# Kernel optimization log

Measured on AMD Instinct MI355X. Metric: run time of the kernel, lower is better.

Reference implementation:

```python
import jax, jax.numpy as jnp
import numpy as np

B, N, T = 512, 24, 25
IN, L, H, OUT = 8, 64, 256, 128


def quat_mul(q, r):
    w1, x1, y1, z1 = jnp.split(q, 4, -1)
    w2, x2, y2, z2 = jnp.split(r, 4, -1)
    return jnp.concatenate([
        w1 * w2 - x1 * x2 - y1 * y2 - z1 * z2,
        w1 * x2 + x1 * w2 + y1 * z2 - z1 * y2,
        w1 * y2 - x1 * z2 + y1 * w2 + z1 * x2,
        w1 * z2 + x1 * y2 - y1 * x2 + z1 * w2], -1)


def node_linear(x, W, b, G):
    # per-node weights [N,F,O], then graph-influence mixing G[N,N]
    y = jnp.einsum('bnf,nfo->bno', x, W) + b
    return jnp.einsum('mn,bno->bmo', G, y)


def graph_linear(x, W, b, G):
    # shared weights [F,O], then graph-influence mixing
    y = jnp.einsum('bnf,fo->bno', x, W) + b
    return jnp.einsum('mn,bno->bmo', G, y)


def lstm_step(x, h, c, Wx, Wh, b, G):
    gates = jnp.einsum('bnf,nfo->bno', x, Wx) + jnp.einsum('bnf,nfo->bno', h, Wh) + b
    gates = jnp.einsum('mn,bno->bmo', G, gates)
    i, f, g, o = jnp.split(gates, 4, -1)
    c = jax.nn.sigmoid(f) * c + jax.nn.sigmoid(i) * jnp.tanh(g)
    h = jax.nn.sigmoid(o) * jnp.tanh(c)
    return h, c


def _p(key, shape, scale):
    return jax.random.normal(key, shape, jnp.float32) * scale


def setup_inputs() -> dict:
    key = jax.random.key(0)
    ks = jax.random.split(key, 20)
    in0 = L + IN
    inp = {
        'x': jax.random.normal(ks[0], (B, 1, N, IN), jnp.float32),
        'enc': jax.random.normal(ks[1], (B, 1, N, H), jnp.float32),
        'z': jax.random.normal(ks[2], (B, 1, N, L), jnp.float32),
        'y': jax.random.normal(ks[3], (B, T, N, 4), jnp.float32),
        'G': jnp.eye(N, dtype=jnp.float32) + 0.02 * jax.random.normal(ks[4], (N, N), jnp.float32),
        'Wx0': _p(ks[5], (N, in0, 4 * OUT), in0 ** -0.5),
        'Wh0': _p(ks[6], (N, OUT, 4 * OUT), OUT ** -0.5),
        'b0': jnp.zeros((N, 4 * OUT), jnp.float32),
        'Wx1': _p(ks[7], (N, OUT, 4 * OUT), OUT ** -0.5),
        'Wh1': _p(ks[8], (N, OUT, 4 * OUT), OUT ** -0.5),
        'b1': jnp.zeros((N, 4 * OUT), jnp.float32),
        'fc_W': _p(ks[9], (N, OUT, OUT), OUT ** -0.5),
        'fc_b': jnp.zeros((N, OUT), jnp.float32),
        'fc2_W': _p(ks[10], (N, OUT, OUT), OUT ** -0.5),
        'fc2_b': jnp.zeros((N, OUT), jnp.float32),
        'ih1_W': _p(ks[11], (H, OUT), H ** -0.5),
        'ih1_b': jnp.zeros((OUT,), jnp.float32),
        'ih2_W': _p(ks[12], (H, OUT), H ** -0.5),
        'ih2_b': jnp.zeros((OUT,), jnp.float32),
        'loc_W': _p(ks[13], (OUT, 3), OUT ** -0.5),
        'loc_b': jnp.zeros((3,), jnp.float32),
        'logz_W': _p(ks[14], (OUT, 4), OUT ** -0.5),
        'logz_b': jnp.zeros((4,), jnp.float32),
    }
    return inp


def reference(x, enc, z, y, G, Wx0, Wh0, b0, Wx1, Wh1, b1, fc_W, fc_b, fc2_W, fc2_b,
              ih1_W, ih1_b, ih2_W, ih2_b, loc_W, loc_b, logz_W, logz_b):
    # eval mode: dropout = identity, no teacher forcing (y unused); rnn2/xi2 are dead code.
    xs, zs, encs = x[:, 0], z[:, 0], enc[:, 0]          # [B,N,*]
    h0 = graph_linear(encs, ih1_W, ih1_b, G)            # shared initial h for both layers
    c0 = graph_linear(encs, ih2_W, ih2_b, G)            # shared initial c for both layers
    loc_start0 = xs[..., :4]
    xi0 = jnp.concatenate([zs, xs], -1)                 # [B,N,L+IN]

    def step(carry, _):
        xi, loc_start, h1, c1, h2, c2 = carry
        h1, c1 = lstm_step(xi, h1, c1, Wx0, Wh0, b0, G)
        h2, c2 = lstm_step(h1, h2, c2, Wx1, Wh1, b1, G)
        yi = jnp.tanh(h2)
        yi1 = jnp.tanh(node_linear(yi, fc_W, fc_b, G))
        yi2 = jnp.tanh(node_linear(yi, fc2_W, fc2_b, G))
        loc3 = graph_linear(yi1, loc_W, loc_b, G)       # [B,N,3]
        log_Z = graph_linear(yi2, logz_W, logz_b, G)    # [B,N,4]
        w = jnp.ones(loc3.shape[:-1] + (1,), loc3.dtype)
        loc4 = jnp.concatenate([w, loc3], -1)
        loc_d = loc4 * jax.lax.rsqrt(jnp.sum(loc4 * loc4, -1, keepdims=True))  # validate
        loc = quat_mul(loc_start, loc_d)                # state_representation.sum
        xi_next = jnp.concatenate([zs, loc, loc_d], -1)
        return (xi_next, loc, h1, c1, h2, c2), (loc, log_Z)

    _, (locs, logzs) = jax.lax.scan(step, (xi0, loc_start0, h0, c0, h0, c0), None, length=T)
    out = jnp.moveaxis(locs, 0, 1)[:, :, None]          # [B,T,1,N,4]
    out_log_diag = jnp.moveaxis(logzs, 0, 1)[:, :, None]
    return out, out_log_diag
```

## Files before the change

kernel.cpp:

```cpp
#include <hip/hip_runtime.h>
#include <math.h>

#define Bsz 512
#define Nn  24
#define Tt  25

typedef _Float16 f16;
typedef _Float16 f16x8 __attribute__((ext_vector_type(8)));
typedef _Float16 f16x4 __attribute__((ext_vector_type(4)));
typedef float f32x4 __attribute__((ext_vector_type(4)));

template <int FN>
__global__ __launch_bounds__(256) void gemm_mfma(
    const f16* __restrict__ Act, const float* __restrict__ Act32, int Ka,
    const f16* __restrict__ W, size_t wstride,
    const float* __restrict__ bias, int bstride,
    const f16* __restrict__ base16,
    f16* __restrict__ Y, int O)
{
    const int BN = FN * 32;
    const int n  = blockIdx.z;
    const int o0 = blockIdx.x * 64;
    const int b0 = blockIdx.y * BN;
    const int tid  = threadIdx.x;
    const int wave = tid >> 6, lane = tid & 63;
    const int wm = (wave >> 1) * 32;
    const int wn = (wave & 1) * FN * 16;
    const int m16 = lane & 15, quad = lane >> 4;

    __shared__ __attribute__((aligned(16))) f16 sW[64][72];
    __shared__ __attribute__((aligned(16))) f16 sB[BN][72];

    const f16* Wn = W + (size_t)n * wstride;
    f32x4 acc[2][FN] = {};
    const int r = tid >> 3, cc = (tid & 7) * 8;

    for (int k0 = 0; k0 < Ka; k0 += 64) {
        for (int row = r; row < 64; row += 32)
            *(f16x8*)&sW[row][cc] = *(const f16x8*)&Wn[(size_t)(o0 + row) * Ka + k0 + cc];
        if (Act) {
            for (int row = r; row < BN; row += 32)
                *(f16x8*)&sB[row][cc] = *(const f16x8*)&Act[((size_t)(b0 + row) * Nn + n) * Ka + k0 + cc];
        } else {
            for (int row = r; row < BN; row += 32) {
                const float* src = &Act32[((size_t)(b0 + row) * Nn + n) * Ka + k0 + cc];
                f16x8 v;
#pragma unroll
                for (int u = 0; u < 8; u++) v[u] = (f16)src[u];
                *(f16x8*)&sB[row][cc] = v;
            }
        }
        __syncthreads();
#pragma unroll
        for (int kk = 0; kk < 64; kk += 32) {
            f16x8 af[2], bf[FN];
#pragma unroll
            for (int i = 0; i < 2; i++)
                af[i] = *(const f16x8*)&sW[wm + i * 16 + m16][kk + quad * 8];
#pragma unroll
            for (int j = 0; j < FN; j++)
                bf[j] = *(const f16x8*)&sB[wn + j * 16 + m16][kk + quad * 8];
#pragma unroll
            for (int i = 0; i < 2; i++)
#pragma unroll
                for (int j = 0; j < FN; j++)
                    acc[i][j] = __builtin_amdgcn_mfma_f32_16x16x32_f16(af[i], bf[j], acc[i][j], 0, 0, 0);
        }
        __syncthreads();
    }
#pragma unroll
    for (int i = 0; i < 2; i++) {
        const int orow = o0 + wm + i * 16 + quad * 4;
        float4 bv = make_float4(0.f, 0.f, 0.f, 0.f);
        if (bias) bv = *(const float4*)&bias[(size_t)n * bstride + orow];
#pragma unroll
        for (int j = 0; j < FN; j++) {
            const int bcol = b0 + wn + j * 16 + m16;
            size_t yi = ((size_t)bcol * Nn + n) * (size_t)O + orow;
            float v0 = acc[i][j][0] + bv.x;
            float v1 = acc[i][j][1] + bv.y;
            float v2 = acc[i][j][2] + bv.z;
            float v3 = acc[i][j][3] + bv.w;
            if (base16) {
                f16x4 bb = *(const f16x4*)&base16[yi];
                v0 += (float)bb[0]; v1 += (float)bb[1];
                v2 += (float)bb[2]; v3 += (float)bb[3];
            }
            f16x4 o4; o4[0] = (f16)v0; o4[1] = (f16)v1; o4[2] = (f16)v2; o4[3] = (f16)v3;
            *(f16x4*)&Y[yi] = o4;
        }
    }
}

__global__ __launch_bounds__(256) void prep_w01(
    const float* __restrict__ Wx0, const float* __restrict__ Wh0,
    const float* __restrict__ Wx1, const float* __restrict__ Wh1,
    f16* __restrict__ Wz, f16* __restrict__ Wt0, f16* __restrict__ W2ext,
    f16* __restrict__ W8)
{
    size_t idx = (size_t)blockIdx.x * 256 + threadIdx.x;
    const size_t nz = (size_t)Nn * 512 * 64;
    const size_t n0 = (size_t)Nn * 512 * 192;
    const size_t n2 = (size_t)Nn * 1024 * 256;
    const size_t n8 = (size_t)Nn * 8 * 512;
    if (idx < nz) {
        int k = idx & 63; int o = (idx >> 6) & 511; int n = (int)(idx >> 15);
        Wz[idx] = (f16)Wx0[((size_t)n * 72 + k) * 512 + o];
    } else if (idx < nz + n0) {
        size_t i2 = idx - nz;
        int k = (int)(i2 % 192);
        size_t no = i2 / 192;
        int o = (int)(no & 511); int n = (int)(no >> 9);
        float v = 0.f;
        if (k < 8) v = Wx0[((size_t)n * 72 + 64 + k) * 512 + o];
        else if (k < 136) v = Wh0[((size_t)n * 128 + (k - 8)) * 512 + o];
        Wt0[i2] = (f16)v;
    } else if (idx < nz + n0 + n2) {
        size_t i3 = idx - nz - n0;
        int k = (int)(i3 & 255);
        size_t no = i3 >> 8;
        int o = (int)(no & 1023); int n = (int)(no >> 10);
        float v;
        if (o < 512) v = (k < 128) ? Wx1[((size_t)n * 128 + k) * 512 + o]
                                   : Wh1[((size_t)n * 128 + (k - 128)) * 512 + o];
        else         v = (k < 128) ? Wh0[((size_t)n * 128 + k) * 512 + (o - 512)] : 0.f;
        W2ext[i3] = (f16)v;
    } else if (idx < nz + n0 + n2 + n8) {
        size_t i4 = idx - nz - n0 - n2;
        int o = (int)(i4 & 511);
        size_t ko = i4 >> 9;
        int k = (int)(ko & 7); int n = (int)(ko >> 3);
        W8[i4] = (f16)Wx0[((size_t)n * 72 + 64 + k) * 512 + o];
    }
}

__global__ __launch_bounds__(256) void prep_wf(
    const float* __restrict__ fcW, const float* __restrict__ fc2W,
    f16* __restrict__ Wtf)
{
    size_t idx = (size_t)blockIdx.x * 256 + threadIdx.x;
    if (idx >= (size_t)Nn * 256 * 128) return;
    int k = (int)(idx & 127);
    size_t no = idx >> 7;
    int o = (int)(no & 255); int n = (int)(no >> 8);
    float v = (o < 128) ? fcW[((size_t)n * 128 + k) * 128 + o]
                        : fc2W[((size_t)n * 128 + k) * 128 + (o - 128)];
    Wtf[idx] = (f16)v;
}

__global__ __launch_bounds__(256) void prep_wi(
    const float* __restrict__ ih1W, const float* __restrict__ ih2W,
    const float* __restrict__ ih1b, const float* __restrict__ ih2b,
    const float* __restrict__ fcb, const float* __restrict__ fc2b,
    const float* __restrict__ b1,
    f16* __restrict__ Wti, float* __restrict__ bi, float* __restrict__ bcat,
    float* __restrict__ bcat2)
{
    int idx = blockIdx.x * 256 + threadIdx.x;
    int k = idx & 255, o = idx >> 8;
    Wti[idx] = (f16)((o < 128) ? ih1W[(size_t)k * 128 + o] : ih2W[(size_t)k * 128 + (o - 128)]);
    if (idx < 256) bi[idx] = (idx < 128) ? ih1b[idx] : ih2b[idx - 128];
    if (idx < Nn * 256) {
        int n = idx >> 8, oo = idx & 255;
        bcat[idx] = (oo < 128) ? fcb[n * 128 + oo] : fc2b[n * 128 + (oo - 128)];
    }
    if (idx < Nn * 1024) {
        int n = idx >> 10, oo = idx & 1023;
        bcat2[idx] = (oo < 512) ? b1[n * 512 + oo] : 0.f;
    }
}

__global__ __launch_bounds__(256) void init_xi(
    const float* __restrict__ x, f16* __restrict__ xi2, float* __restrict__ ls)
{
    size_t idx = (size_t)blockIdx.x * 256 + threadIdx.x;
    const size_t total = (size_t)Bsz * Nn * 192;
    if (idx < total) {
        size_t bn = idx / 192;
        int k = (int)(idx - bn * 192);
        if (k < 8) xi2[idx] = (f16)x[bn * 8 + k];
        else if (k >= 136) xi2[idx] = (f16)0.f;
    }
    if (idx < (size_t)Bsz * Nn * 4) {
        size_t bn = idx >> 2;
        ls[idx] = x[bn * 8 + (idx & 3)];
    }
}

__global__ __launch_bounds__(256) void mix_init(
    const f16* __restrict__ Yhc, const float* __restrict__ G,
    f16* __restrict__ xi2, f16* __restrict__ l2cat,
    float* __restrict__ c1, float* __restrict__ c2)
{
    const int b = blockIdx.x;
    const int tid = threadIdx.x;
    __shared__ float sY[6144], sG[576];
    for (int i = tid; i < 576; i += 256) sG[i] = G[i];
    for (int v = tid; v < 768; v += 256) {
        int c8 = (v & 31) * 8, n = v >> 5;
        f16x8 t = *(const f16x8*)&Yhc[((size_t)b * Nn + n) * 256 + c8];
        float* d = &sY[n * 256 + c8];
#pragma unroll
        for (int u = 0; u < 8; u++) d[u] = (float)t[u];
    }
    __syncthreads();
    for (int w = tid; w < 3072; w += 256) {
        int o = w & 127, m = w >> 7;
        float ah = 0.f, ac = 0.f;
#pragma unroll
        for (int n = 0; n < 24; n++) {
            float g = sG[m * 24 + n];
            ah += g * sY[n * 256 + o];
            ac += g * sY[n * 256 + 128 + o];
        }
        size_t row = (size_t)b * Nn + m;
        f16 hf = (f16)ah;
        xi2[row * 192 + 8 + o] = hf;
        l2cat[row * 256 + o] = hf;
        l2cat[row * 256 + 128 + o] = hf;
        c1[row * 128 + o] = ac;
        c2[row * 128 + o] = ac;
    }
}

__global__ __launch_bounds__(256) void mixlstm_b(
    const f16* __restrict__ Ypre, int ystride, const float* __restrict__ G,
    float* __restrict__ c,
    f16* __restrict__ dstA, int strideA,
    f16* __restrict__ dstB, int strideB)
{
    const int b = blockIdx.x;
    const int tid = threadIdx.x;
    __shared__ __attribute__((aligned(16))) f16 sY[12288];
    __shared__ float sG[576];
    for (int i = tid; i < 576; i += 256) sG[i] = G[i];
    for (int i = tid; i < 1536; i += 256) {
        int n = i >> 6, c8 = (i & 63) * 8;
        *(f16x8*)&sY[n * 512 + c8] = *(const f16x8*)&Ypre[((size_t)b * Nn + n) * ystride + c8];
    }
    __syncthreads();
    for (int w = tid; w < 768; w += 256) {
        const int m = w >> 5, j4 = (w & 31) * 4;
        float gi[4] = {}, gf[4] = {}, gg[4] = {}, go[4] = {};
        const float* gr = &sG[m * 24];
#pragma unroll
        for (int n = 0; n < 24; n++) {
            float g = gr[n];
            const f16* yn = &sY[n * 512];
            f16x4 vi = *(const f16x4*)&yn[j4];
            f16x4 vf = *(const f16x4*)&yn[128 + j4];
            f16x4 vg = *(const f16x4*)&yn[256 + j4];
            f16x4 vo = *(const f16x4*)&yn[384 + j4];
#pragma unroll
            for (int u = 0; u < 4; u++) {
                gi[u] += g * (float)vi[u];
                gf[u] += g * (float)vf[u];
                gg[u] += g * (float)vg[u];
                go[u] += g * (float)vo[u];
            }
        }
        const size_t row = (size_t)b * Nn + m;
        float cv[4];
        *(float4*)cv = *(const float4*)&c[row * 128 + j4];
        f16x4 ha, hb;
#pragma unroll
        for (int u = 0; u < 4; u++) {
            float si = 1.f / (1.f + expf(-gi[u]));
            float sf = 1.f / (1.f + expf(-gf[u]));
            float so = 1.f / (1.f + expf(-go[u]));
            float cn = sf * cv[u] + si * tanhf(gg[u]);
            cv[u] = cn;
            float h = so * tanhf(cn);
            ha[u] = (f16)h;
            hb[u] = (f16)tanhf(h);
        }
        *(float4*)&c[row * 128 + j4] = *(float4*)cv;
        *(f16x4*)&dstA[row * strideA + j4] = ha;
        if (dstB) *(f16x4*)&dstB[row * strideB + j4] = hb;
    }
}

__global__ __launch_bounds__(256) void finstep(
    const f16* __restrict__ p, const f16* __restrict__ ypB,
    const f16* __restrict__ base1, const f16* __restrict__ W8,
    const float* __restrict__ G,
    const float* __restrict__ locW, const float* __restrict__ locb,
    const float* __restrict__ lzW, const float* __restrict__ lzb,
    float* __restrict__ ls, f16* __restrict__ ypA,
    float* __restrict__ out, int t)
{
    const int b = blockIdx.x;
    const int tid = threadIdx.x;
    __shared__ __attribute__((aligned(16))) f16 sP[6144];
    __shared__ __attribute__((aligned(16))) f16 sY1[3072], sY2[3072];
    __shared__ float sG[576];
    __shared__ float sLp[24][3], sZp[24][4], sL3[24][3], sZ3[24][4];
    __shared__ float sV8[24][8];
    for (int i = tid; i < 576; i += 256) sG[i] = G[i];
    for (int i = tid; i < 768; i += 256) {
        int n = i >> 5, c8 = (i & 31) * 8;
        *(f16x8*)&sP[n * 256 + c8] = *(const f16x8*)&p[((size_t)b * Nn + n) * 256 + c8];
    }
    __syncthreads();
    for (int w = tid; w < 768; w += 256) {
        const int m = w >> 5, o4 = (w & 31) * 4;
        float a1[4] = {}, a2[4] = {};
        const float* gr = &sG[m * 24];
#pragma unroll
        for (int n = 0; n < 24; n++) {
            float g = gr[n];
            f16x4 p1 = *(const f16x4*)&sP[n * 256 + o4];
            f16x4 p2 = *(const f16x4*)&sP[n * 256 + 128 + o4];
#pragma unroll
            for (int u = 0; u < 4; u++) { a1[u] += g * (float)p1[u]; a2[u] += g * (float)p2[u]; }
        }
        f16x4 y1, y2;
#pragma unroll
        for (int u = 0; u < 4; u++) { y1[u] = (f16)tanhf(a1[u]); y2[u] = (f16)tanhf(a2[u]); }
        *(f16x4*)&sY1[m * 128 + o4] = y1;
        *(f16x4*)&sY2[m * 128 + o4] = y2;
    }
    __syncthreads();
    if (tid < 72) {
        int m = tid / 3, j = tid - m * 3;
        float s = locb[j];
        for (int o = 0; o < 128; o++) s += (float)sY1[m * 128 + o] * locW[o * 3 + j];
        sLp[m][j] = s;
    } else if (tid < 168) {
        int w2 = tid - 72; int m = w2 >> 2, j = w2 & 3;
        float s = lzb[j];
        for (int o = 0; o < 128; o++) s += (float)sY2[m * 128 + o] * lzW[o * 4 + j];
        sZp[m][j] = s;
    }
    __syncthreads();
    if (tid < 72) {
        int m = tid / 3, j = tid - m * 3;
        float s = 0.f;
#pragma unroll
        for (int n = 0; n < 24; n++) s += sG[m * 24 + n] * sLp[n][j];
        sL3[m][j] = s;
    } else if (tid < 168) {
        int w2 = tid - 72; int m = w2 >> 2, j = w2 & 3;
        float s = 0.f;
#pragma unroll
        for (int n = 0; n < 24; n++) s += sG[m * 24 + n] * sZp[n][j];
        sZ3[m][j] = s;
    }
    __syncthreads();
    if (tid < 24) {
        const int m = tid;
        float xx = sL3[m][0], xy = sL3[m][1], xz = sL3[m][2];
        float r = rsqrtf(1.f + xx * xx + xy * xy + xz * xz);
        float dw = r, dx = xx * r, dy = xy * r, dz = xz * r;
        size_t li = ((size_t)b * Nn + m) * 4;
        float qw = ls[li], qx = ls[li + 1], qy = ls[li + 2], qz = ls[li + 3];
        float lw = qw * dw - qx * dx - qy * dy - qz * dz;
        float lx = qw * dx + qx * dw + qy * dz - qz * dy;
        float ly = qw * dy - qx * dz + qy * dw + qz * dx;
        float lz = qw * dz + qx * dy - qy * dx + qz * dw;
        size_t oi = (((size_t)b * Tt + t) * Nn + m) * 4;
        out[oi + 0] = lw; out[oi + 1] = lx; out[oi + 2] = ly; out[oi + 3] = lz;
        size_t zi = (size_t)Bsz * Tt * Nn * 4 + oi;
        out[zi + 0] = sZ3[m][0]; out[zi + 1] = sZ3[m][1];
        out[zi + 2] = sZ3[m][2]; out[zi + 3] = sZ3[m][3];
        ls[li] = lw; ls[li + 1] = lx; ls[li + 2] = ly; ls[li + 3] = lz;
        sV8[m][0] = lw; sV8[m][1] = lx; sV8[m][2] = ly; sV8[m][3] = lz;
        sV8[m][4] = dw; sV8[m][5] = dx; sV8[m][6] = dy; sV8[m][7] = dz;
    }
    __syncthreads();
    for (int g = tid; g < 1536; g += 256) {
        const int n = g >> 6, o8 = (g & 63) * 8;
        const size_t rowb = (size_t)b * Nn + n;
        f16x8 pp = *(const f16x8*)&ypB[rowb * 1024 + 512 + o8];
        f16x8 bb = *(const f16x8*)&base1[rowb * 512 + o8];
        float acc[8];
#pragma unroll
        for (int u = 0; u < 8; u++) acc[u] = (float)pp[u] + (float)bb[u];
#pragma unroll
        for (int k = 0; k < 8; k++) {
            float v = sV8[n][k];
            f16x8 ww = *(const f16x8*)&W8[((size_t)n * 8 + k) * 512 + o8];
#pragma unroll
            for (int u = 0; u < 8; u++) acc[u] += v * (float)ww[u];
        }
        f16x8 oo;
#pragma unroll
        for (int u = 0; u < 8; u++) oo[u] = (f16)acc[u];
        *(f16x8*)&ypA[rowb * 512 + o8] = oo;
    }
}

extern "C" void kernel_launch(void* const* d_in, const int* in_sizes, int n_in,
                              void* d_out, int out_size, void* d_ws, size_t ws_size,
                              hipStream_t stream)
{
    const float* x    = (const float*)d_in[0];
    const float* enc  = (const float*)d_in[1];
    const float* z    = (const float*)d_in[2];
    const float* G    = (const float*)d_in[4];
    const float* Wx0  = (const float*)d_in[5];
    const float* Wh0  = (const float*)d_in[6];
    const float* b0i  = (const float*)d_in[7];
    const float* Wx1  = (const float*)d_in[8];
    const float* Wh1  = (const float*)d_in[9];
    const float* b1i  = (const float*)d_in[10];
    const float* fcW  = (const float*)d_in[11];
    const float* fcb  = (const float*)d_in[12];
    const float* fc2W = (const float*)d_in[13];
    const float* fc2b = (const float*)d_in[14];
    const float* ih1W = (const float*)d_in[15];
    const float* ih1b = (const float*)d_in[16];
    const float* ih2W = (const float*)d_in[17];
    const float* ih2b = (const float*)d_in[18];
    const float* locW = (const float*)d_in[19];
    const float* locb = (const float*)d_in[20];
    const float* lzW  = (const float*)d_in[21];
    const float* lzb  = (const float*)d_in[22];
    float* out = (float*)d_out;

    const size_t BN = (size_t)Bsz * Nn;
    char* wp = (char*)d_ws;
    size_t off = 0;
    auto carve = [&](size_t bytes) -> char* {
        char* pc = wp + off;
        off += (bytes + 255) & ~(size_t)255;
        return pc;
    };
    f16*   Wz     = (f16*)carve((size_t)Nn * 512 * 64 * 2);
    f16*   Wt0    = (f16*)carve((size_t)Nn * 512 * 192 * 2);
    f16*   W2ext  = (f16*)carve((size_t)Nn * 1024 * 256 * 2);
    f16*   W8     = (f16*)carve((size_t)Nn * 8 * 512 * 2);
    f16*   Wtf    = (f16*)carve((size_t)Nn * 256 * 128 * 2);
    f16*   Wti    = (f16*)carve((size_t)256 * 256 * 2);
    float* bcat   = (float*)carve((size_t)Nn * 256 * 4);
    float* bcat2  = (float*)carve((size_t)Nn * 1024 * 4);
    float* bi     = (float*)carve(256 * 4);
    f16*   base1  = (f16*)carve(BN * 512 * 2);
    f16*   xi2    = (f16*)carve(BN * 192 * 2);
    f16*   l2cat  = (f16*)carve(BN * 256 * 2);
    f16*   yib    = (f16*)carve(BN * 128 * 2);
    float* c1     = (float*)carve(BN * 128 * 4);
    float* c2     = (float*)carve(BN * 128 * 4);
    float* ls     = (float*)carve(BN * 4 * 4);
    f16*   ypA    = (f16*)carve(BN * 512 * 2);
    f16*   ypB    = (f16*)carve(BN * 1024 * 2);
    f16*   yp0    = (f16*)carve(BN * 256 * 2);
    f16*   pbuf   = (f16*)carve(BN * 256 * 2);

    prep_w01<<<37248, 256, 0, stream>>>(Wx0, Wh0, Wx1, Wh1, Wz, Wt0, W2ext, W8);
    prep_wf<<<3072, 256, 0, stream>>>(fcW, fc2W, Wtf);
    prep_wi<<<256, 256, 0, stream>>>(ih1W, ih2W, ih1b, ih2b, fcb, fc2b, b1i,
                                     Wti, bi, bcat, bcat2);
    init_xi<<<9216, 256, 0, stream>>>(x, xi2, ls);

    gemm_mfma<4><<<dim3(8, 4, 24), 256, 0, stream>>>(
        nullptr, z, 64, Wz, (size_t)512 * 64, b0i, 512, nullptr, base1, 512);
    gemm_mfma<4><<<dim3(4, 4, 24), 256, 0, stream>>>(
        nullptr, enc, 256, Wti, 0, bi, 0, nullptr, yp0, 256);
    mix_init<<<512, 256, 0, stream>>>(yp0, G, xi2, l2cat, c1, c2);
    gemm_mfma<4><<<dim3(8, 4, 24), 256, 0, stream>>>(
        xi2, nullptr, 192, Wt0, (size_t)512 * 192, nullptr, 0, base1, ypA, 512);

    for (int t = 0; t < Tt; t++) {
        mixlstm_b<<<512, 256, 0, stream>>>(ypA, 512, G, c1, l2cat, 256, nullptr, 0);
        gemm_mfma<8><<<dim3(16, 2, 24), 256, 0, stream>>>(
            l2cat, nullptr, 256, W2ext, (size_t)1024 * 256, bcat2, 1024, nullptr, ypB, 1024);
        mixlstm_b<<<512, 256, 0, stream>>>(ypB, 1024, G, c2, l2cat + 128, 256, yib, 128);
        gemm_mfma<4><<<dim3(4, 4, 24), 256, 0, stream>>>(
            yib, nullptr, 128, Wtf, (size_t)256 * 128, bcat, 256, nullptr, pbuf, 256);
        finstep<<<512, 256, 0, stream>>>(pbuf, ypB, base1, W8, G, locW, locb, lzW, lzb,
                                         ls, ypA, out, t);
    }
}
```

Baseline: 2.661 ms.

## Use 128x128 GEMM tiles, move layer-0 gate assembly into the mix kernel

```diff
diff --git a/kernel.cpp b/kernel.cpp
--- a/kernel.cpp
+++ b/kernel.cpp
@@ -10,39 +10,38 @@
 typedef _Float16 f16x4 __attribute__((ext_vector_type(4)));
 typedef float f32x4 __attribute__((ext_vector_type(4)));
 
-template <int FN>
-__global__ __launch_bounds__(256) void gemm_mfma(
+__global__ __launch_bounds__(256) void gemm128(
     const f16* __restrict__ Act, const float* __restrict__ Act32, int Ka,
-    const f16* __restrict__ W, size_t wstride,
+    const f16* __restrict__ W, size_t wstride, int otiles, int bpn,
     const float* __restrict__ bias, int bstride,
-    const f16* __restrict__ base16,
-    f16* __restrict__ Y, int O)
-{
-    const int BN = FN * 32;
-    const int n  = blockIdx.z;
-    const int o0 = blockIdx.x * 64;
-    const int b0 = blockIdx.y * BN;
+    f16* __restrict__ Y, int ystride, int yoff)
+{
+    const int bid = blockIdx.x;
+    const int n     = (bid & 7) + 8 * (bid / (8 * bpn));
+    const int inner = (bid >> 3) % bpn;
+    const int o0 = (inner % otiles) * 128;
+    const int b0 = (inner / otiles) * 128;
     const int tid  = threadIdx.x;
     const int wave = tid >> 6, lane = tid & 63;
-    const int wm = (wave >> 1) * 32;
-    const int wn = (wave & 1) * FN * 16;
+    const int wm = (wave >> 1) * 64;
+    const int wn = (wave & 1) * 64;
     const int m16 = lane & 15, quad = lane >> 4;
 
-    __shared__ __attribute__((aligned(16))) f16 sW[64][72];
-    __shared__ __attribute__((aligned(16))) f16 sB[BN][72];
+    __shared__ __attribute__((aligned(16))) f16 sW[128][72];
+    __shared__ __attribute__((aligned(16))) f16 sB[128][72];
 
     const f16* Wn = W + (size_t)n * wstride;
-    f32x4 acc[2][FN] = {};
+    f32x4 acc[4][4] = {};
     const int r = tid >> 3, cc = (tid & 7) * 8;
 
     for (int k0 = 0; k0 < Ka; k0 += 64) {
-        for (int row = r; row < 64; row += 32)
+        for (int row = r; row < 128; row += 32)
             *(f16x8*)&sW[row][cc] = *(const f16x8*)&Wn[(size_t)(o0 + row) * Ka + k0 + cc];
         if (Act) {
-            for (int row = r; row < BN; row += 32)
+            for (int row = r; row < 128; row += 32)
                 *(f16x8*)&sB[row][cc] = *(const f16x8*)&Act[((size_t)(b0 + row) * Nn + n) * Ka + k0 + cc];
         } else {
-            for (int row = r; row < BN; row += 32) {
+            for (int row = r; row < 128; row += 32) {
                 const float* src = &Act32[((size_t)(b0 + row) * Nn + n) * Ka + k0 + cc];
                 f16x8 v;
 #pragma unroll
@@ -53,40 +52,35 @@
         __syncthreads();
 #pragma unroll
         for (int kk = 0; kk < 64; kk += 32) {
-            f16x8 af[2], bf[FN];
-#pragma unroll
-            for (int i = 0; i < 2; i++)
+            f16x8 af[4], bf[4];
+#pragma unroll
+            for (int i = 0; i < 4; i++)
                 af[i] = *(const f16x8*)&sW[wm + i * 16 + m16][kk + quad * 8];
 #pragma unroll
-            for (int j = 0; j < FN; j++)
+            for (int j = 0; j < 4; j++)
                 bf[j] = *(const f16x8*)&sB[wn + j * 16 + m16][kk + quad * 8];
 #pragma unroll
-            for (int i = 0; i < 2; i++)
-#pragma unroll
-                for (int j = 0; j < FN; j++)
+            for (int i = 0; i < 4; i++)
+#pragma unroll
+                for (int j = 0; j < 4; j++)
                     acc[i][j] = __builtin_amdgcn_mfma_f32_16x16x32_f16(af[i], bf[j], acc[i][j], 0, 0, 0);
         }
         __syncthreads();
     }
 #pragma unroll
-    for (int i = 0; i < 2; i++) {
+    for (int i = 0; i < 4; i++) {
         const int orow = o0 + wm + i * 16 + quad * 4;
         float4 bv = make_float4(0.f, 0.f, 0.f, 0.f);
         if (bias) bv = *(const float4*)&bias[(size_t)n * bstride + orow];
 #pragma unroll
-        for (int j = 0; j < FN; j++) {
+        for (int j = 0; j < 4; j++) {
             const int bcol = b0 + wn + j * 16 + m16;
-            size_t yi = ((size_t)bcol * Nn + n) * (size_t)O + orow;
-            float v0 = acc[i][j][0] + bv.x;
-            float v1 = acc[i][j][1] + bv.y;
-            float v2 = acc[i][j][2] + bv.z;
-            float v3 = acc[i][j][3] + bv.w;
-            if (base16) {
-                f16x4 bb = *(const f16x4*)&base16[yi];
-                v0 += (float)bb[0]; v1 += (float)bb[1];
-                v2 += (float)bb[2]; v3 += (float)bb[3];
-            }
-            f16x4 o4; o4[0] = (f16)v0; o4[1] = (f16)v1; o4[2] = (f16)v2; o4[3] = (f16)v3;
+            size_t yi = ((size_t)bcol * Nn + n) * (size_t)ystride + yoff + orow;
+            f16x4 o4;
+            o4[0] = (f16)(acc[i][j][0] + bv.x);
+            o4[1] = (f16)(acc[i][j][1] + bv.y);
+            o4[2] = (f16)(acc[i][j][2] + bv.z);
+            o4[3] = (f16)(acc[i][j][3] + bv.w);
             *(f16x4*)&Y[yi] = o4;
         }
     }
@@ -95,28 +89,19 @@
 __global__ __launch_bounds__(256) void prep_w01(
     const float* __restrict__ Wx0, const float* __restrict__ Wh0,
     const float* __restrict__ Wx1, const float* __restrict__ Wh1,
-    f16* __restrict__ Wz, f16* __restrict__ Wt0, f16* __restrict__ W2ext,
-    f16* __restrict__ W8)
+    f16* __restrict__ Wz, f16* __restrict__ W2ext, f16* __restrict__ W8,
+    f16* __restrict__ Wh0t)
 {
     size_t idx = (size_t)blockIdx.x * 256 + threadIdx.x;
     const size_t nz = (size_t)Nn * 512 * 64;
-    const size_t n0 = (size_t)Nn * 512 * 192;
     const size_t n2 = (size_t)Nn * 1024 * 256;
     const size_t n8 = (size_t)Nn * 8 * 512;
+    const size_t nh = (size_t)Nn * 512 * 128;
     if (idx < nz) {
         int k = idx & 63; int o = (idx >> 6) & 511; int n = (int)(idx >> 15);
         Wz[idx] = (f16)Wx0[((size_t)n * 72 + k) * 512 + o];
-    } else if (idx < nz + n0) {
-        size_t i2 = idx - nz;
-        int k = (int)(i2 % 192);
-        size_t no = i2 / 192;
-        int o = (int)(no & 511); int n = (int)(no >> 9);
-        float v = 0.f;
-        if (k < 8) v = Wx0[((size_t)n * 72 + 64 + k) * 512 + o];
-        else if (k < 136) v = Wh0[((size_t)n * 128 + (k - 8)) * 512 + o];
-        Wt0[i2] = (f16)v;
-    } else if (idx < nz + n0 + n2) {
-        size_t i3 = idx - nz - n0;
+    } else if (idx < nz + n2) {
+        size_t i3 = idx - nz;
         int k = (int)(i3 & 255);
         size_t no = i3 >> 8;
         int o = (int)(no & 1023); int n = (int)(no >> 10);
@@ -125,12 +110,18 @@
                                    : Wh1[((size_t)n * 128 + (k - 128)) * 512 + o];
         else         v = (k < 128) ? Wh0[((size_t)n * 128 + k) * 512 + (o - 512)] : 0.f;
         W2ext[i3] = (f16)v;
-    } else if (idx < nz + n0 + n2 + n8) {
-        size_t i4 = idx - nz - n0 - n2;
+    } else if (idx < nz + n2 + n8) {
+        size_t i4 = idx - nz - n2;
         int o = (int)(i4 & 511);
         size_t ko = i4 >> 9;
         int k = (int)(ko & 7); int n = (int)(ko >> 3);
         W8[i4] = (f16)Wx0[((size_t)n * 72 + 64 + k) * 512 + o];
+    } else if (idx < nz + n2 + n8 + nh) {
+        size_t i5 = idx - nz - n2 - n8;
+        int k = (int)(i5 & 127);
+        size_t no = i5 >> 7;
+        int o = (int)(no & 511); int n = (int)(no >> 9);
+        Wh0t[i5] = (f16)Wh0[((size_t)n * 128 + k) * 512 + o];
     }
 }
 
@@ -170,26 +161,22 @@
     }
 }
 
-__global__ __launch_bounds__(256) void init_xi(
-    const float* __restrict__ x, f16* __restrict__ xi2, float* __restrict__ ls)
+__global__ __launch_bounds__(256) void init_small(
+    const float* __restrict__ x, f16* __restrict__ v8f, float* __restrict__ ls)
 {
     size_t idx = (size_t)blockIdx.x * 256 + threadIdx.x;
-    const size_t total = (size_t)Bsz * Nn * 192;
-    if (idx < total) {
-        size_t bn = idx / 192;
-        int k = (int)(idx - bn * 192);
-        if (k < 8) xi2[idx] = (f16)x[bn * 8 + k];
-        else if (k >= 136) xi2[idx] = (f16)0.f;
-    }
-    if (idx < (size_t)Bsz * Nn * 4) {
-        size_t bn = idx >> 2;
-        ls[idx] = x[bn * 8 + (idx & 3)];
+    if (idx < (size_t)Bsz * Nn * 8) {
+        v8f[idx] = (f16)x[idx];
+        if ((idx & 7) < 4) {
+            size_t bn = idx >> 3;
+            ls[bn * 4 + (idx & 3)] = x[idx];
+        }
     }
 }
 
 __global__ __launch_bounds__(256) void mix_init(
     const f16* __restrict__ Yhc, const float* __restrict__ G,
-    f16* __restrict__ xi2, f16* __restrict__ l2cat,
+    f16* __restrict__ h0f, f16* __restrict__ l2cat,
     float* __restrict__ c1, float* __restrict__ c2)
 {
     const int b = blockIdx.x;
@@ -215,19 +202,102 @@
         }
         size_t row = (size_t)b * Nn + m;
         f16 hf = (f16)ah;
-        xi2[row * 192 + 8 + o] = hf;
-        l2cat[row * 256 + o] = hf;
+        h0f[row * 128 + o] = hf;
         l2cat[row * 256 + 128 + o] = hf;
         c1[row * 128 + o] = ac;
         c2[row * 128 + o] = ac;
     }
 }
 
-__global__ __launch_bounds__(256) void mixlstm_b(
-    const f16* __restrict__ Ypre, int ystride, const float* __restrict__ G,
+__global__ __launch_bounds__(256) void mix1c(
+    const f16* __restrict__ ypB, const f16* __restrict__ base1,
+    const f16* __restrict__ W8, const f16* __restrict__ v8f,
+    const float* __restrict__ G,
+    float* __restrict__ c1, f16* __restrict__ l2cat)
+{
+    const int bg = blockIdx.x >> 2;
+    const int jt = (blockIdx.x & 3) * 32;
+    const int b0 = bg * 8;
+    const int tid = threadIdx.x;
+    __shared__ __attribute__((aligned(16))) f16 sYc[8][24][136];
+    __shared__ float sG[576];
+    __shared__ __attribute__((aligned(16))) f16 sV8[8][24][8];
+    for (int i = tid; i < 576; i += 256) sG[i] = G[i];
+    for (int i = tid; i < 192; i += 256) {
+        int bb = i / 24, n = i - bb * 24;
+        *(f16x8*)&sV8[bb][n][0] = *(const f16x8*)&v8f[((size_t)(b0 + bb) * Nn + n) * 8];
+    }
+    __syncthreads();
+    for (int i = tid; i < 3072; i += 256) {
+        const int c8 = (i & 15) * 8;
+        const int n  = (i >> 4) % 24;
+        const int bb = (i >> 4) / 24;
+        const int g = c8 >> 5;
+        const int o8 = g * 128 + jt + (c8 & 31);
+        const size_t rowb = (size_t)(b0 + bb) * Nn + n;
+        f16x8 pp = *(const f16x8*)&ypB[rowb * 1024 + 512 + o8];
+        f16x8 bs = *(const f16x8*)&base1[rowb * 512 + o8];
+        float acc[8];
+#pragma unroll
+        for (int u = 0; u < 8; u++) acc[u] = (float)pp[u] + (float)bs[u];
+#pragma unroll
+        for (int k = 0; k < 8; k++) {
+            float v = (float)sV8[bb][n][k];
+            f16x8 ww = *(const f16x8*)&W8[((size_t)n * 8 + k) * 512 + o8];
+#pragma unroll
+            for (int u = 0; u < 8; u++) acc[u] += v * (float)ww[u];
+        }
+        f16x8 oo;
+#pragma unroll
+        for (int u = 0; u < 8; u++) oo[u] = (f16)acc[u];
+        *(f16x8*)&sYc[bb][n][c8] = oo;
+    }
+    __syncthreads();
+    for (int w = tid; w < 1536; w += 256) {
+        const int j4 = (w & 7) * 4;
+        const int m  = (w >> 3) % 24;
+        const int bb = (w >> 3) / 24;
+        float gi[4] = {}, gf[4] = {}, gg[4] = {}, go[4] = {};
+        const float* gr = &sG[m * 24];
+#pragma unroll
+        for (int n = 0; n < 24; n++) {
+            float g = gr[n];
+            const f16* yn = &sYc[bb][n][0];
+            f16x4 vi = *(const f16x4*)&yn[j4];
+            f16x4 vf = *(const f16x4*)&yn[32 + j4];
+            f16x4 vg = *(const f16x4*)&yn[64 + j4];
+            f16x4 vo = *(const f16x4*)&yn[96 + j4];
+#pragma unroll
+            for (int u = 0; u < 4; u++) {
+                gi[u] += g * (float)vi[u];
+                gf[u] += g * (float)vf[u];
+                gg[u] += g * (float)vg[u];
+                go[u] += g * (float)vo[u];
+            }
+        }
+        const size_t row = (size_t)(b0 + bb) * Nn + m;
+        const int col = jt + j4;
+        float cv[4];
+        *(float4*)cv = *(const float4*)&c1[row * 128 + col];
+        f16x4 ha;
+#pragma unroll
+        for (int u = 0; u < 4; u++) {
+            float si = 1.f / (1.f + expf(-gi[u]));
+            float sf = 1.f / (1.f + expf(-gf[u]));
+            float so = 1.f / (1.f + expf(-go[u]));
+            float cn = sf * cv[u] + si * tanhf(gg[u]);
+            cv[u] = cn;
+            ha[u] = (f16)(so * tanhf(cn));
+        }
+        *(float4*)&c1[row * 128 + col] = *(float4*)cv;
+        *(f16x4*)&l2cat[row * 256 + col] = ha;
+    }
+}
+
+__global__ __launch_bounds__(256) void mix2(
+    const f16* __restrict__ ypB, const float* __restrict__ G,
     float* __restrict__ c,
-    f16* __restrict__ dstA, int strideA,
-    f16* __restrict__ dstB, int strideB)
+    f16* __restrict__ dstA, f16* __restrict__ dstB)
 {
     const int b = blockIdx.x;
     const int tid = threadIdx.x;
@@ -236,7 +306,7 @@
     for (int i = tid; i < 576; i += 256) sG[i] = G[i];
     for (int i = tid; i < 1536; i += 256) {
         int n = i >> 6, c8 = (i & 63) * 8;
-        *(f16x8*)&sY[n * 512 + c8] = *(const f16x8*)&Ypre[((size_t)b * Nn + n) * ystride + c8];
+        *(f16x8*)&sY[n * 512 + c8] = *(const f16x8*)&ypB[((size_t)b * Nn + n) * 1024 + c8];
     }
     __syncthreads();
     for (int w = tid; w < 768; w += 256) {
@@ -275,18 +345,16 @@
             hb[u] = (f16)tanhf(h);
         }
         *(float4*)&c[row * 128 + j4] = *(float4*)cv;
-        *(f16x4*)&dstA[row * strideA + j4] = ha;
-        if (dstB) *(f16x4*)&dstB[row * strideB + j4] = hb;
+        *(f16x4*)&dstA[row * 256 + 128 + j4] = ha;
+        *(f16x4*)&dstB[row * 128 + j4] = hb;
     }
 }
 
 __global__ __launch_bounds__(256) void finstep(
-    const f16* __restrict__ p, const f16* __restrict__ ypB,
-    const f16* __restrict__ base1, const f16* __restrict__ W8,
-    const float* __restrict__ G,
+    const f16* __restrict__ p, const float* __restrict__ G,
     const float* __restrict__ locW, const float* __restrict__ locb,
     const float* __restrict__ lzW, const float* __restrict__ lzb,
-    float* __restrict__ ls, f16* __restrict__ ypA,
+    float* __restrict__ ls, f16* __restrict__ v8f,
     float* __restrict__ out, int t)
 {
     const int b = blockIdx.x;
@@ -295,7 +363,6 @@
     __shared__ __attribute__((aligned(16))) f16 sY1[3072], sY2[3072];
     __shared__ float sG[576];
     __shared__ float sLp[24][3], sZp[24][4], sL3[24][3], sZ3[24][4];
-    __shared__ float sV8[24][8];
     for (int i = tid; i < 576; i += 256) sG[i] = G[i];
     for (int i = tid; i < 768; i += 256) {
         int n = i >> 5, c8 = (i & 31) * 8;
@@ -364,29 +431,10 @@
         out[zi + 0] = sZ3[m][0]; out[zi + 1] = sZ3[m][1];
         out[zi + 2] = sZ3[m][2]; out[zi + 3] = sZ3[m][3];
         ls[li] = lw; ls[li + 1] = lx; ls[li + 2] = ly; ls[li + 3] = lz;
-        sV8[m][0] = lw; sV8[m][1] = lx; sV8[m][2] = ly; sV8[m][3] = lz;
-        sV8[m][4] = dw; sV8[m][5] = dx; sV8[m][6] = dy; sV8[m][7] = dz;
-    }
-    __syncthreads();
-    for (int g = tid; g < 1536; g += 256) {
-        const int n = g >> 6, o8 = (g & 63) * 8;
-        const size_t rowb = (size_t)b * Nn + n;
-        f16x8 pp = *(const f16x8*)&ypB[rowb * 1024 + 512 + o8];
-        f16x8 bb = *(const f16x8*)&base1[rowb * 512 + o8];
-        float acc[8];
-#pragma unroll
-        for (int u = 0; u < 8; u++) acc[u] = (float)pp[u] + (float)bb[u];
-#pragma unroll
-        for (int k = 0; k < 8; k++) {
-            float v = sV8[n][k];
-            f16x8 ww = *(const f16x8*)&W8[((size_t)n * 8 + k) * 512 + o8];
-#pragma unroll
-            for (int u = 0; u < 8; u++) acc[u] += v * (float)ww[u];
-        }
-        f16x8 oo;
-#pragma unroll
-        for (int u = 0; u < 8; u++) oo[u] = (f16)acc[u];
-        *(f16x8*)&ypA[rowb * 512 + o8] = oo;
+        f16x8 v8;
+        v8[0] = (f16)lw; v8[1] = (f16)lx; v8[2] = (f16)ly; v8[3] = (f16)lz;
+        v8[4] = (f16)dw; v8[5] = (f16)dx; v8[6] = (f16)dy; v8[7] = (f16)dz;
+        *(f16x8*)&v8f[((size_t)b * Nn + m) * 8] = v8;
     }
 }
 
@@ -427,48 +475,47 @@
         return pc;
     };
     f16*   Wz     = (f16*)carve((size_t)Nn * 512 * 64 * 2);
-    f16*   Wt0    = (f16*)carve((size_t)Nn * 512 * 192 * 2);
     f16*   W2ext  = (f16*)carve((size_t)Nn * 1024 * 256 * 2);
     f16*   W8     = (f16*)carve((size_t)Nn * 8 * 512 * 2);
+    f16*   Wh0t   = (f16*)carve((size_t)Nn * 512 * 128 * 2);
     f16*   Wtf    = (f16*)carve((size_t)Nn * 256 * 128 * 2);
     f16*   Wti    = (f16*)carve((size_t)256 * 256 * 2);
     float* bcat   = (float*)carve((size_t)Nn * 256 * 4);
     float* bcat2  = (float*)carve((size_t)Nn * 1024 * 4);
     float* bi     = (float*)carve(256 * 4);
     f16*   base1  = (f16*)carve(BN * 512 * 2);
-    f16*   xi2    = (f16*)carve(BN * 192 * 2);
     f16*   l2cat  = (f16*)carve(BN * 256 * 2);
     f16*   yib    = (f16*)carve(BN * 128 * 2);
+    f16*   h0f    = (f16*)carve(BN * 128 * 2);
     float* c1     = (float*)carve(BN * 128 * 4);
     float* c2     = (float*)carve(BN * 128 * 4);
     float* ls     = (float*)carve(BN * 4 * 4);
-    f16*   ypA    = (f16*)carve(BN * 512 * 2);
+    f16*   v8f    = (f16*)carve(BN * 8 * 2);
     f16*   ypB    = (f16*)carve(BN * 1024 * 2);
     f16*   yp0    = (f16*)carve(BN * 256 * 2);
     f16*   pbuf   = (f16*)carve(BN * 256 * 2);
 
-    prep_w01<<<37248, 256, 0, stream>>>(Wx0, Wh0, Wx1, Wh1, Wz, Wt0, W2ext, W8);
+    prep_w01<<<34176, 256, 0, stream>>>(Wx0, Wh0, Wx1, Wh1, Wz, W2ext, W8, Wh0t);
     prep_wf<<<3072, 256, 0, stream>>>(fcW, fc2W, Wtf);
     prep_wi<<<256, 256, 0, stream>>>(ih1W, ih2W, ih1b, ih2b, fcb, fc2b, b1i,
                                      Wti, bi, bcat, bcat2);
-    init_xi<<<9216, 256, 0, stream>>>(x, xi2, ls);
-
-    gemm_mfma<4><<<dim3(8, 4, 24), 256, 0, stream>>>(
-        nullptr, z, 64, Wz, (size_t)512 * 64, b0i, 512, nullptr, base1, 512);
-    gemm_mfma<4><<<dim3(4, 4, 24), 256, 0, stream>>>(
-        nullptr, enc, 256, Wti, 0, bi, 0, nullptr, yp0, 256);
-    mix_init<<<512, 256, 0, stream>>>(yp0, G, xi2, l2cat, c1, c2);
-    gemm_mfma<4><<<dim3(8, 4, 24), 256, 0, stream>>>(
-        xi2, nullptr, 192, Wt0, (size_t)512 * 192, nullptr, 0, base1, ypA, 512);
+    init_small<<<384, 256, 0, stream>>>(x, v8f, ls);
+
+    gemm128<<<384, 256, 0, stream>>>(nullptr, z, 64, Wz, (size_t)512 * 64, 4, 16,
+                                     b0i, 512, base1, 512, 0);
+    gemm128<<<192, 256, 0, stream>>>(nullptr, enc, 256, Wti, 0, 2, 8,
+                                     bi, 0, yp0, 256, 0);
+    mix_init<<<512, 256, 0, stream>>>(yp0, G, h0f, l2cat, c1, c2);
+    gemm128<<<384, 256, 0, stream>>>(h0f, nullptr, 128, Wh0t, (size_t)512 * 128, 4, 16,
+                                     nullptr, 0, ypB, 1024, 512);
 
     for (int t = 0; t < Tt; t++) {
-        mixlstm_b<<<512, 256, 0, stream>>>(ypA, 512, G, c1, l2cat, 256, nullptr, 0);
-        gemm_mfma<8><<<dim3(16, 2, 24), 256, 0, stream>>>(
-            l2cat, nullptr, 256, W2ext, (size_t)1024 * 256, bcat2, 1024, nullptr, ypB, 1024);
-        mixlstm_b<<<512, 256, 0, stream>>>(ypB, 1024, G, c2, l2cat + 128, 256, yib, 128);
-        gemm_mfma<4><<<dim3(4, 4, 24), 256, 0, stream>>>(
-            yib, nullptr, 128, Wtf, (size_t)256 * 128, bcat, 256, nullptr, pbuf, 256);
-        finstep<<<512, 256, 0, stream>>>(pbuf, ypB, base1, W8, G, locW, locb, lzW, lzb,
-                                         ls, ypA, out, t);
-    }
-}
+        mix1c<<<256, 256, 0, stream>>>(ypB, base1, W8, v8f, G, c1, l2cat);
+        gemm128<<<768, 256, 0, stream>>>(l2cat, nullptr, 256, W2ext, (size_t)1024 * 256,
+                                         8, 32, bcat2, 1024, ypB, 1024, 0);
+        mix2<<<512, 256, 0, stream>>>(ypB, G, c2, l2cat, yib);
+        gemm128<<<192, 256, 0, stream>>>(yib, nullptr, 128, Wtf, (size_t)256 * 128,
+                                         2, 8, bcat, 256, pbuf, 256, 0);
+        finstep<<<512, 256, 0, stream>>>(pbuf, G, locW, locb, lzW, lzb, ls, v8f, out, t);
+    }
+}
```

Measured after the change: 2.698 ms. No clear change (+1.4%).
